# Kernel optimization log

Hardware: AMD Instinct MI355X
Metric: run time of the kernel (lower is better)

The kernel has to match this reference:

```python
import jax, jax.numpy as jnp
import numpy as np

N = 8192      # total packed vision tokens
D = 1280      # hidden_size
H = 16        # num_heads
K = 80        # head_dim = D // H
M = 16        # number of image segments
LMAX = 1024   # static upper bound on per-image segment length
SCALE = K ** (-0.5)
NEG = -1e30   # finite mask value (avoids NaN on fully-padded rows)


def _rotate_half(x):
    h = x.shape[-1] // 2
    return jnp.concatenate([-x[..., h:], x[..., :h]], axis=-1)


def setup_inputs() -> dict:
    key = jax.random.key(0)
    ks = jax.random.split(key, 5)
    hidden = jax.random.normal(ks[0], (N, D), jnp.float32)
    # ragged per-image lengths (sum == N, each <= LMAX)
    lengths = np.array([256, 768] * (M // 2), dtype=np.int32)
    cu = jnp.asarray(np.concatenate([[0], np.cumsum(lengths)]).astype(np.int32))
    # rotary tables, shape (N, head_dim)
    inv_freq = 1.0 / (10000.0 ** (np.arange(0, K, 2, dtype=np.float32) / K))  # (K/2,)
    freqs = np.arange(N, dtype=np.float32)[:, None] * inv_freq[None, :]       # (N, K/2)
    emb = np.concatenate([freqs, freqs], axis=-1)                              # (N, K)
    cos = jnp.asarray(np.cos(emb), jnp.float32)
    sin = jnp.asarray(np.sin(emb), jnp.float32)
    W_qkv = jax.random.normal(ks[1], (D, 3 * D), jnp.float32) * (D ** -0.5)
    b_qkv = jax.random.normal(ks[2], (3 * D,), jnp.float32) * 0.01
    W_proj = jax.random.normal(ks[3], (D, D), jnp.float32) * (D ** -0.5)
    b_proj = jax.random.normal(ks[4], (D,), jnp.float32) * 0.01
    return dict(hidden_ND=hidden, cu_seqlens=cu, cos_NK=cos, sin_NK=sin,
                W_qkv=W_qkv, b_qkv=b_qkv, W_proj=W_proj, b_proj=b_proj)


def reference(hidden_ND, cu_seqlens, cos_NK, sin_NK, W_qkv, b_qkv, W_proj, b_proj):
    n = hidden_ND.shape[0]
    # fused QKV projection
    qkv = (hidden_ND @ W_qkv + b_qkv).reshape(n, 3, H, K)
    q, k, v = qkv[:, 0], qkv[:, 1], qkv[:, 2]          # (N, H, K)
    # inline RoPE on Q/K (fp32 math, as in apply_rotary_pos_emb_vision)
    cos = cos_NK[:, None, :]
    sin = sin_NK[:, None, :]
    q = q * cos + _rotate_half(q) * sin
    k = k * cos + _rotate_half(k) * sin
    # gather packed tokens into padded per-segment blocks (honors segment sparsity:
    # no cross-segment tiles are ever materialized)
    lengths = jnp.diff(cu_seqlens)                                  # (M,)
    idx = cu_seqlens[:-1, None] + jnp.arange(LMAX)[None, :]         # (M, LMAX)
    valid = jnp.arange(LMAX)[None, :] < lengths[:, None]            # (M, LMAX)
    idxc = jnp.minimum(idx, n - 1)
    qg, kg, vg = q[idxc], k[idxc], v[idxc]                          # (M, LMAX, H, K)
    # per-segment attention
    scores = jnp.einsum('mqhd,mkhd->mhqk', qg, kg) * SCALE          # (M, H, LMAX, LMAX)
    mask = valid[:, None, :, None] & valid[:, None, None, :]
    scores = jnp.where(mask, scores, NEG)
    p = jax.nn.softmax(scores, axis=-1)
    og = jnp.einsum('mhqk,mkhd->mqhd', p, vg)                       # (M, LMAX, H, K)
    # scatter back to packed layout: token n -> (segment, position)
    seg = jnp.searchsorted(cu_seqlens[1:], jnp.arange(n), side='right')
    pos = jnp.arange(n) - cu_seqlens[seg]
    attn_ND = og[seg, pos].reshape(n, H * K)
    return attn_ND @ W_proj + b_proj
```

## Files before the change

kernel.cpp:

```cpp
#include <hip/hip_runtime.h>
#include <hip/hip_bf16.h>
#include <stdint.h>

#define NTOK 8192
#define DMODEL 1280
#define NHEAD 16
#define HDIM 80
#define NSEG 16
#define SCALE_F 0.11180339887498949f
#define NEG_F -1e30f

typedef __bf16 bf16x8 __attribute__((ext_vector_type(8)));
typedef float f32x4 __attribute__((ext_vector_type(4)));

__device__ __forceinline__ void gload_lds16(const void* g, void* l) {
  __builtin_amdgcn_global_load_lds((__attribute__((address_space(1))) void*)g,
                                   (__attribute__((address_space(3))) void*)l,
                                   16, 0, 0);
}

__global__ __launch_bounds__(256)
void cvt_f32_to_bf16(const float* __restrict__ src, __hip_bfloat16* __restrict__ dst) {
  int i = (blockIdx.x * 256 + threadIdx.x) * 4;
  float4 v = *(const float4*)(src + i);
  __align__(8) __hip_bfloat16 o[4] = {__float2bfloat16(v.x), __float2bfloat16(v.y),
                                      __float2bfloat16(v.z), __float2bfloat16(v.w)};
  *(uint2*)(dst + i) = *(const uint2*)o;
}

__global__ __launch_bounds__(256)
void transpose_w(const float* __restrict__ src, __hip_bfloat16* __restrict__ dst,
                 int R, int C) {
  __shared__ __hip_bfloat16 tile[32][33];
  int c0 = blockIdx.x * 32, r0 = blockIdx.y * 32;
  int tx = threadIdx.x & 31, ty = threadIdx.x >> 5;
#pragma unroll
  for (int i = 0; i < 4; ++i) {
    int r = ty + i * 8;
    tile[r][tx] = __float2bfloat16(src[(size_t)(r0 + r) * C + c0 + tx]);
  }
  __syncthreads();
#pragma unroll
  for (int i = 0; i < 4; ++i) {
    int r = ty + i * 8;
    dst[(size_t)(c0 + r) * R + r0 + tx] = tile[tx][r];
  }
}

__global__ __launch_bounds__(256)
void rope2(__hip_bfloat16* __restrict__ qkv,
           const float* __restrict__ cosb, const float* __restrict__ sinb) {
  int t = blockIdx.x * 256 + threadIdx.x;
  int p = t % 5;
  int rest = t / 5;
  int h = rest & 15;
  int qk = (rest >> 4) & 1;
  int n = rest >> 5;
  size_t base = (size_t)n * 3840 + qk * 1280 + h * 80 + p * 8;
  const float* cb = cosb + n * 80 + p * 8;
  const float* sb = sinb + n * 80 + p * 8;
  float4 cA = *(const float4*)cb, cB = *(const float4*)(cb + 4);
  float4 cC = *(const float4*)(cb + 40), cD = *(const float4*)(cb + 44);
  float4 sA = *(const float4*)sb, sB = *(const float4*)(sb + 4);
  float4 sC = *(const float4*)(sb + 40), sD = *(const float4*)(sb + 44);
  float c0[8] = {cA.x, cA.y, cA.z, cA.w, cB.x, cB.y, cB.z, cB.w};
  float c1[8] = {cC.x, cC.y, cC.z, cC.w, cD.x, cD.y, cD.z, cD.w};
  float s0[8] = {sA.x, sA.y, sA.z, sA.w, sB.x, sB.y, sB.z, sB.w};
  float s1[8] = {sC.x, sC.y, sC.z, sC.w, sD.x, sD.y, sD.z, sD.w};
  uint4 lou = *(const uint4*)(qkv + base);
  uint4 hiu = *(const uint4*)(qkv + base + 40);
  __align__(16) __hip_bfloat16 lo[8], hh[8], olo[8], ohi[8];
  *(uint4*)lo = lou; *(uint4*)hh = hiu;
#pragma unroll
  for (int e = 0; e < 8; ++e) {
    float x0 = __bfloat162float(lo[e]);
    float x1 = __bfloat162float(hh[e]);
    olo[e] = __float2bfloat16(x0 * c0[e] - x1 * s0[e]);
    ohi[e] = __float2bfloat16(x1 * c1[e] + x0 * s1[e]);
  }
  *(uint4*)(qkv + base) = *(const uint4*)olo;
  *(uint4*)(qkv + base + 40) = *(const uint4*)ohi;
}

template <bool OUT_F32, bool A_F32>
__global__ __launch_bounds__(256)
void gemm128(const void* __restrict__ Av, int lda,
             const __hip_bfloat16* __restrict__ Bt,
             const float* __restrict__ bias,
             void* __restrict__ Cv, int M, int N, int K) {
  __shared__ __align__(16) __hip_bfloat16 lds[8192];
  const int tid = threadIdx.x;
  const int lane = tid & 63;
  const int wave = tid >> 6;
  const int wr = wave >> 1, wc = wave & 1;
  const int lr = lane & 15;
  const int hi = lane >> 4;
  const int sw = (lr >> 1) & 3;
  const int lk = (hi ^ sw) << 3;
  const int m0 = blockIdx.x * 128;
  const int n0 = blockIdx.y * 128;

  f32x4 zero = {0.f, 0.f, 0.f, 0.f};
  f32x4 acc[4][4];
#pragma unroll
  for (int i = 0; i < 4; ++i)
#pragma unroll
    for (int j = 0; j < 4; ++j) acc[i][j] = zero;

  for (int k0 = 0; k0 < K; k0 += 32) {
#pragma unroll
    for (int j = 0; j < 2; ++j) {
      int v = j * 256 + tid;
      int row = v >> 2;
      int cb = ((v & 3) ^ ((v >> 3) & 3)) << 3;
      gload_lds16(Bt + (size_t)(n0 + row) * K + k0 + cb,
                  &lds[4096 + wave * 512 + j * 2048]);
    }
    if constexpr (A_F32) {
      const float* A32 = (const float*)Av;
      float4 vv[4];
#pragma unroll
      for (int j = 0; j < 4; ++j) {
        int task = j * 256 + tid;
        int row = task >> 3, cc = task & 7;
        vv[j] = *(const float4*)(A32 + (size_t)(m0 + row) * lda + k0 + cc * 4);
      }
#pragma unroll
      for (int j = 0; j < 4; ++j) {
        int task = j * 256 + tid;
        int row = task >> 3, cc = task & 7;
        int s = (cc >> 1) ^ ((row >> 1) & 3);
        __align__(8) __hip_bfloat16 t[4] = {
            __float2bfloat16(vv[j].x), __float2bfloat16(vv[j].y),
            __float2bfloat16(vv[j].z), __float2bfloat16(vv[j].w)};
        *(uint2*)&lds[row * 32 + s * 8 + (cc & 1) * 4] = *(const uint2*)t;
      }
    } else {
      const __hip_bfloat16* Abf = (const __hip_bfloat16*)Av;
#pragma unroll
      for (int j = 0; j < 2; ++j) {
        int v = j * 256 + tid;
        int row = v >> 2;
        int cb = ((v & 3) ^ ((v >> 3) & 3)) << 3;
        gload_lds16(Abf + (size_t)(m0 + row) * lda + k0 + cb,
                    &lds[wave * 512 + j * 2048]);
      }
    }
    __syncthreads();

    bf16x8 af[4], bfr[4];
#pragma unroll
    for (int i = 0; i < 4; ++i) {
      af[i]  = *(const bf16x8*)&lds[(wr * 64 + i * 16 + lr) * 32 + lk];
      bfr[i] = *(const bf16x8*)&lds[4096 + (wc * 64 + i * 16 + lr) * 32 + lk];
    }
#pragma unroll
    for (int i = 0; i < 4; ++i)
#pragma unroll
      for (int j = 0; j < 4; ++j)
        acc[i][j] = __builtin_amdgcn_mfma_f32_16x16x32_bf16(af[i], bfr[j], acc[i][j], 0, 0, 0);
    __syncthreads();
  }

  const int r0 = (lane >> 4) << 2;
#pragma unroll
  for (int j = 0; j < 4; ++j) {
    int col = n0 + wc * 64 + j * 16 + lr;
    float bv = bias[col];
#pragma unroll
    for (int i = 0; i < 4; ++i) {
      int rowb = m0 + wr * 64 + i * 16 + r0;
#pragma unroll
      for (int r = 0; r < 4; ++r) {
        float val = acc[i][j][r] + bv;
        if (OUT_F32)
          ((float*)Cv)[(size_t)(rowb + r) * N + col] = val;
        else
          ((__hip_bfloat16*)Cv)[(size_t)(rowb + r) * N + col] = __float2bfloat16(val);
      }
    }
  }
}

__global__ __launch_bounds__(512, 2)
void gemm256(const __hip_bfloat16* __restrict__ A,
             const __hip_bfloat16* __restrict__ Bt,
             const float* __restrict__ bias,
             __hip_bfloat16* __restrict__ C, int M, int N, int K) {
  __shared__ __align__(16) __hip_bfloat16 lds[49152];
  const int tid = threadIdx.x;
  const int lane = tid & 63;
  const int wave = tid >> 6;
  const int wr = wave >> 2;
  const int wc = wave & 3;
  const int lr = lane & 15;
  const int hi = lane >> 4;
  const int sw = (lr >> 1) & 3;
  const int lk = (hi ^ sw) << 3;
  const int m0 = blockIdx.x * 256;
  const int n0 = blockIdx.y * 256;

  const int scol = ((tid & 3) ^ ((tid >> 3) & 3)) * 8;
  const __hip_bfloat16* srcA = A + (size_t)(m0 + (tid >> 2)) * K + scol;
  const __hip_bfloat16* srcB = Bt + (size_t)(n0 + (tid >> 2)) * K + scol;
  const size_t row128 = (size_t)128 * K;

  auto stageA = [&](int kt, int b) {
    const __hip_bfloat16* s = srcA + kt * 32;
    gload_lds16(s,          &lds[b * 16384 + tid * 8]);
    gload_lds16(s + row128, &lds[b * 16384 + 4096 + tid * 8]);
  };
  auto stageB = [&](int kt, int b) {
    const __hip_bfloat16* s = srcB + kt * 32;
    gload_lds16(s,          &lds[b * 16384 + 8192 + tid * 8]);
    gload_lds16(s + row128, &lds[b * 16384 + 8192 + 4096 + tid * 8]);
  };

  f32x4 acc[8][4];
  f32x4 fz = {0.f, 0.f, 0.f, 0.f};
#pragma unroll
  for (int i = 0; i < 8; ++i)
#pragma unroll
    for (int j = 0; j < 4; ++j) acc[i][j] = fz;

  const int nkt = K >> 5;
  stageA(0, 0); stageB(0, 0);
  stageA(1, 1); stageB(1, 1);
  asm volatile("s_waitcnt vmcnt(4)" ::: "memory");
  __builtin_amdgcn_sched_barrier(0);
  __builtin_amdgcn_s_barrier();

  for (int t = 0; t < nkt; ++t) {
    const int b = t % 3;
    const int bs = (t + 2) % 3;
    const int ktn = (t + 2 < nkt) ? t + 2 : nkt - 1;
    const __hip_bfloat16* Ab = &lds[b * 16384 + (wr * 128) * 32];
    const __hip_bfloat16* Bb = &lds[b * 16384 + 8192 + (wc * 64) * 32];

    bf16x8 bf[4], af[4];
#pragma unroll
    for (int j = 0; j < 4; ++j) bf[j] = *(const bf16x8*)&Bb[(j * 16 + lr) * 32 + lk];
#pragma unroll
    for (int i = 0; i < 4; ++i) af[i] = *(const bf16x8*)&Ab[(i * 16 + lr) * 32 + lk];
    stageA(ktn, bs);
    __builtin_amdgcn_sched_barrier(0);
    __builtin_amdgcn_s_barrier();
    asm volatile("s_waitcnt lgkmcnt(0)" ::: "memory");
    __builtin_amdgcn_sched_barrier(0);
    __builtin_amdgcn_s_setprio(1);
#pragma unroll
    for (int i = 0; i < 4; ++i)
#pragma unroll
      for (int j = 0; j < 4; ++j)
        acc[i][j] = __builtin_amdgcn_mfma_f32_16x16x32_bf16(af[i], bf[j], acc[i][j], 0, 0, 0);
    __builtin_amdgcn_s_setprio(0);
    __builtin_amdgcn_sched_barrier(0);
    __builtin_amdgcn_s_barrier();

#pragma unroll
    for (int i = 0; i < 4; ++i) af[i] = *(const bf16x8*)&Ab[((i + 4) * 16 + lr) * 32 + lk];
    stageB(ktn, bs);
    asm volatile("s_waitcnt vmcnt(4)" ::: "memory");
    __builtin_amdgcn_sched_barrier(0);
    __builtin_amdgcn_s_barrier();
    asm volatile("s_waitcnt lgkmcnt(0)" ::: "memory");
    __builtin_amdgcn_sched_barrier(0);
    __builtin_amdgcn_s_setprio(1);
#pragma unroll
    for (int i = 0; i < 4; ++i)
#pragma unroll
      for (int j = 0; j < 4; ++j)
        acc[4 + i][j] = __builtin_amdgcn_mfma_f32_16x16x32_bf16(af[i], bf[j], acc[4 + i][j], 0, 0, 0);
    __builtin_amdgcn_s_setprio(0);
    __builtin_amdgcn_sched_barrier(0);
    __builtin_amdgcn_s_barrier();
  }

#pragma unroll
  for (int j = 0; j < 4; ++j) {
    int col = n0 + wc * 64 + j * 16 + lr;
    float bv = bias[col];
#pragma unroll
    for (int i = 0; i < 8; ++i) {
      int row0 = m0 + wr * 128 + i * 16 + hi * 4;
#pragma unroll
      for (int r = 0; r < 4; ++r)
        C[(size_t)(row0 + r) * N + col] = __float2bfloat16(acc[i][j][r] + bv);
    }
  }
}

__global__ __launch_bounds__(256, 3)
void attn_fwd(__hip_bfloat16* __restrict__ qkv, const int* __restrict__ cu) {
  const int bid = blockIdx.x;
  const int l = (bid & 7) * 288 + (bid >> 3);
  const int h = l / 144;
  const int pid = l - h * 144;
  int seg = -1, qt = 0, start = 0, L = 0;
  int accq = 0;
#pragma unroll 1
  for (int s2 = 0; s2 < NSEG; ++s2) {
    int st = cu[s2], en = cu[s2 + 1];
    int len = en - st;
    int nq = (len + 63) >> 6;
    if (seg < 0 && pid < accq + nq) { seg = s2; qt = pid - accq; start = st; L = len; }
    accq += nq;
  }
  if (seg < 0) return;

  __shared__ __align__(16) __hip_bfloat16 Ks[2][64 * 80];
  __shared__ __align__(16) __hip_bfloat16 Vs[2][80 * 72];
  __shared__ __align__(16) __hip_bfloat16 Ps[4][16 * 72];

  const int tid = threadIdx.x;
  const int lane = tid & 63;
  const int wave = tid >> 6;
  const int lr = lane & 15;
  const int hi = lane >> 4;
  const int lk = hi * 8;
  const int nt = (L + 63) >> 6;

  bf16x8 aq[3];
  {
    bf16x8 z;
#pragma unroll
    for (int e = 0; e < 8; ++e) z[e] = (__bf16)0.0f;
    int qr = qt * 64 + wave * 16 + lr;
    if (qr > L - 1) qr = L - 1;
    const __hip_bfloat16* qp = qkv + (size_t)(start + qr) * 3840 + h * 80;
    bf16x8 a0 = *(const bf16x8*)(qp + lk);
    bf16x8 a1 = *(const bf16x8*)(qp + 32 + lk);
    bf16x8 a2 = (hi < 2) ? *(const bf16x8*)(qp + 64 + lk) : z;
#pragma unroll
    for (int e = 0; e < 8; ++e) {
      a0[e] = (__bf16)((float)a0[e] * SCALE_F);
      a1[e] = (__bf16)((float)a1[e] * SCALE_F);
      a2[e] = (__bf16)((float)a2[e] * SCALE_F);
    }
    aq[0] = a0; aq[1] = a1; aq[2] = a2;
  }

  const __hip_bfloat16* kbase = qkv + (size_t)start * 3840 + 1280 + h * 80;
  const __hip_bfloat16* vbase = qkv + (size_t)start * 3840 + 2560 + h * 80;

  auto stageK = [&](int t, int buf) {
#pragma unroll
    for (int j = 0; j < 3; ++j) {
      int i = wave + 4 * j;
      if (i < 10) {
        int E = i * 512 + lane * 8;
        int r = E / 80;
        int c = E - r * 80;
        int g = t * 64 + r;
        if (g > L - 1) g = L - 1;
        gload_lds16(kbase + (size_t)g * 3840 + c, (char*)&Ks[buf][0] + i * 1024);
      }
    }
  };
  uint4 vr[3];
  auto loadV = [&](int t) {
    int g = t * 64 + lane;
    if (g > L - 1) g = L - 1;
    size_t roff = (size_t)g * 3840;
#pragma unroll
    for (int j = 0; j < 3; ++j) {
      int c = wave + 4 * j;
      if (c < 10) vr[j] = *(const uint4*)(vbase + roff + c * 8);
    }
  };
  auto writeV = [&](int buf) {
#pragma unroll
    for (int j = 0; j < 3; ++j) {
      int c = wave + 4 * j;
      if (c < 10) {
        __align__(16) __hip_bfloat16 tmp[8];
        *(uint4*)tmp = vr[j];
#pragma unroll
        for (int e = 0; e < 8; ++e) Vs[buf][(c * 8 + e) * 72 + lane] = tmp[e];
      }
    }
  };

  float m_run[4], l_part[4];
  f32x4 fz = {0.f, 0.f, 0.f, 0.f};
  f32x4 accO[5];
#pragma unroll
  for (int r = 0; r < 4; ++r) { m_run[r] = NEG_F; l_part[r] = 0.f; }
#pragma unroll
  for (int d = 0; d < 5; ++d) accO[d] = fz;

  stageK(0, 0);
  loadV(0);
  writeV(0);
  loadV(nt > 1 ? 1 : 0);
  __syncthreads();

  int cur = 0;
  for (int t = 0; t < nt; ++t) {
    const bool more = (t + 1 < nt);
    if (more) {
      stageK(t + 1, cur ^ 1);
      writeV(cur ^ 1);
      loadV(t + 2 < nt ? t + 2 : nt - 1);
    }

    f32x4 s[4] = {fz, fz, fz, fz};
#pragma unroll
    for (int ks = 0; ks < 3; ++ks) {
#pragma unroll
      for (int j = 0; j < 4; ++j) {
        bf16x8 bk = *(const bf16x8*)&Ks[cur][(j * 16 + lr) * 80 + ks * 32 + lk];
        s[j] = __builtin_amdgcn_mfma_f32_16x16x32_bf16(aq[ks], bk, s[j], 0, 0, 0);
      }
    }
    if (t * 64 + 64 > L) {
#pragma unroll
      for (int j = 0; j < 4; ++j) {
        bool vj = (t * 64 + j * 16 + lr) < L;
#pragma unroll
        for (int r = 0; r < 4; ++r)
          s[j][r] = vj ? s[j][r] : NEG_F;
      }
    }
    float mx[4];
    bool need = false;
#pragma unroll
    for (int r = 0; r < 4; ++r) {
      mx[r] = fmaxf(fmaxf(s[0][r], s[1][r]), fmaxf(s[2][r], s[3][r]));
      need |= mx[r] > m_run[r] + 8.0f;
    }
    if (__any(need)) {
#pragma unroll
      for (int off = 1; off < 16; off <<= 1)
#pragma unroll
        for (int r = 0; r < 4; ++r)
          mx[r] = fmaxf(mx[r], __shfl_xor(mx[r], off, 64));
#pragma unroll
      for (int r = 0; r < 4; ++r) {
        float mn = fmaxf(m_run[r], mx[r]);
        float sf = __expf(m_run[r] - mn);
        m_run[r] = mn;
        l_part[r] *= sf;
#pragma unroll
        for (int d = 0; d < 5; ++d) accO[d][r] *= sf;
      }
    }
#pragma unroll
    for (int r = 0; r < 4; ++r) {
      float a0 = __expf(s[0][r] - m_run[r]); s[0][r] = a0;
      float a1 = __expf(s[1][r] - m_run[r]); s[1][r] = a1;
      float a2 = __expf(s[2][r] - m_run[r]); s[2][r] = a2;
      float a3 = __expf(s[3][r] - m_run[r]); s[3][r] = a3;
      l_part[r] += (a0 + a1) + (a2 + a3);
    }

    __hip_bfloat16* pw = &Ps[wave][0];
#pragma unroll
    for (int j = 0; j < 4; ++j)
#pragma unroll
      for (int r = 0; r < 4; ++r)
        pw[(hi * 4 + r) * 72 + j * 16 + lr] = __float2bfloat16(s[j][r]);
    asm volatile("s_waitcnt lgkmcnt(0)" ::: "memory");
    __builtin_amdgcn_sched_barrier(0);
    bf16x8 ap0 = *(const bf16x8*)&pw[lr * 72 + lk];
    bf16x8 ap1 = *(const bf16x8*)&pw[lr * 72 + 32 + lk];
#pragma unroll
    for (int d = 0; d < 5; ++d) {
      bf16x8 bv0 = *(const bf16x8*)&Vs[cur][(d * 16 + lr) * 72 + lk];
      bf16x8 bv1 = *(const bf16x8*)&Vs[cur][(d * 16 + lr) * 72 + 32 + lk];
      accO[d] = __builtin_amdgcn_mfma_f32_16x16x32_bf16(ap0, bv0, accO[d], 0, 0, 0);
      accO[d] = __builtin_amdgcn_mfma_f32_16x16x32_bf16(ap1, bv1, accO[d], 0, 0, 0);
    }

    __syncthreads();
    cur ^= 1;
  }

#pragma unroll
  for (int off = 1; off < 16; off <<= 1)
#pragma unroll
    for (int r = 0; r < 4; ++r)
      l_part[r] += __shfl_xor(l_part[r], off, 64);
  float rl[4];
#pragma unroll
  for (int r = 0; r < 4; ++r) rl[r] = 1.0f / l_part[r];
#pragma unroll
  for (int d = 0; d < 5; ++d)
#pragma unroll
    for (int r = 0; r < 4; ++r) {
      int row = qt * 64 + wave * 16 + hi * 4 + r;
      if (row < L)
        qkv[(size_t)(start + row) * 3840 + h * 80 + d * 16 + lr] =
            __float2bfloat16(accO[d][r] * rl[r]);
    }
}

extern "C" void kernel_launch(void* const* d_in, const int* in_sizes, int n_in,
                              void* d_out, int out_size, void* d_ws, size_t ws_size,
                              hipStream_t stream) {
  const float* hidden = (const float*)d_in[0];
  const int*   cu     = (const int*)d_in[1];
  const float* cosb   = (const float*)d_in[2];
  const float* sinb   = (const float*)d_in[3];
  const float* Wqkv   = (const float*)d_in[4];
  const float* bqkv   = (const float*)d_in[5];
  const float* Wproj  = (const float*)d_in[6];
  const float* bproj  = (const float*)d_in[7];
  float* out = (float*)d_out;
  char* ws = (char*)d_ws;

  __hip_bfloat16* qkv    = (__hip_bfloat16*)(ws);
  __hip_bfloat16* wqkvT  = (__hip_bfloat16*)(ws + 62914560);
  __hip_bfloat16* wprojT = (__hip_bfloat16*)(ws + 72744960);
  __hip_bfloat16* hbf    = (__hip_bfloat16*)(ws + 76021760);
  const bool use_hbf = ws_size >= (size_t)96993280;

  transpose_w<<<dim3(120, 40), 256, 0, stream>>>(Wqkv, wqkvT, 1280, 3840);
  transpose_w<<<dim3(40, 40), 256, 0, stream>>>(Wproj, wprojT, 1280, 1280);
  if (use_hbf) {
    cvt_f32_to_bf16<<<10240, 256, 0, stream>>>(hidden, hbf);
    gemm256<<<dim3(32, 15), 512, 0, stream>>>(hbf, wqkvT, bqkv, qkv, 8192, 3840, 1280);
  } else {
    gemm128<false, true><<<dim3(64, 30), 256, 0, stream>>>(hidden, 1280, wqkvT, bqkv, qkv, 8192, 3840, 1280);
  }
  rope2<<<5120, 256, 0, stream>>>(qkv, cosb, sinb);
  attn_fwd<<<2304, 256, 0, stream>>>(qkv, cu);
  gemm128<true, false><<<dim3(64, 10), 256, 0, stream>>>(qkv, 3840, wprojT, bproj, out, 8192, 1280, 1280);
}
```

Baseline: 255.3 us.

## Shrink gemm256 tile to 256x128 with double buffering and reuse it for output projection

Changes the big GEMM kernel from a 256x256 triple-buffered tile to a 256x128 double-buffered tile with a 4x2 wave layout and half the accumulators. This allows four blocks per CU and doubles the grid for the QKV projection. The kernel is templated on output type with an lda parameter so it can also replace gemm128 for the output projection. The goal is better occupancy and latency hiding. The cost is less operand reuse per tile and a full vmcnt(0) wait every k-step, which exposes load latency.

```diff
diff --git a/kernel.cpp b/kernel.cpp
--- a/kernel.cpp
+++ b/kernel.cpp
@@ -182,67 +182,61 @@
   }
 }
 
-__global__ __launch_bounds__(512, 2)
-void gemm256(const __hip_bfloat16* __restrict__ A,
+template <bool OUT_F32>
+__global__ __launch_bounds__(512, 4)
+void gemm256(const __hip_bfloat16* __restrict__ A, int lda,
              const __hip_bfloat16* __restrict__ Bt,
              const float* __restrict__ bias,
-             __hip_bfloat16* __restrict__ C, int M, int N, int K) {
-  __shared__ __align__(16) __hip_bfloat16 lds[49152];
+             void* __restrict__ Cv, int M, int N, int K) {
+  __shared__ __align__(16) __hip_bfloat16 lds[2][12288];
   const int tid = threadIdx.x;
   const int lane = tid & 63;
   const int wave = tid >> 6;
-  const int wr = wave >> 2;
-  const int wc = wave & 3;
+  const int wr = wave >> 1;
+  const int wc = wave & 1;
   const int lr = lane & 15;
   const int hi = lane >> 4;
-  const int sw = (lr >> 1) & 3;
-  const int lk = (hi ^ sw) << 3;
+  const int lk = (hi ^ ((lr >> 1) & 3)) << 3;
   const int m0 = blockIdx.x * 256;
-  const int n0 = blockIdx.y * 256;
+  const int n0 = blockIdx.y * 128;
 
   const int scol = ((tid & 3) ^ ((tid >> 3) & 3)) * 8;
-  const __hip_bfloat16* srcA = A + (size_t)(m0 + (tid >> 2)) * K + scol;
+  const __hip_bfloat16* srcA = A + (size_t)(m0 + (tid >> 2)) * lda + scol;
   const __hip_bfloat16* srcB = Bt + (size_t)(n0 + (tid >> 2)) * K + scol;
-  const size_t row128 = (size_t)128 * K;
-
-  auto stageA = [&](int kt, int b) {
-    const __hip_bfloat16* s = srcA + kt * 32;
-    gload_lds16(s,          &lds[b * 16384 + tid * 8]);
-    gload_lds16(s + row128, &lds[b * 16384 + 4096 + tid * 8]);
+  const size_t rowA128 = (size_t)128 * lda;
+
+  auto stage = [&](int kt, int b) {
+    const __hip_bfloat16* sa = srcA + kt * 32;
+    gload_lds16(sa,           &lds[b][tid * 8]);
+    gload_lds16(sa + rowA128, &lds[b][4096 + tid * 8]);
+    gload_lds16(srcB + kt * 32, &lds[b][8192 + tid * 8]);
   };
-  auto stageB = [&](int kt, int b) {
-    const __hip_bfloat16* s = srcB + kt * 32;
-    gload_lds16(s,          &lds[b * 16384 + 8192 + tid * 8]);
-    gload_lds16(s + row128, &lds[b * 16384 + 8192 + 4096 + tid * 8]);
-  };
-
-  f32x4 acc[8][4];
+
+  f32x4 acc[4][4];
   f32x4 fz = {0.f, 0.f, 0.f, 0.f};
 #pragma unroll
-  for (int i = 0; i < 8; ++i)
+  for (int i = 0; i < 4; ++i)
 #pragma unroll
     for (int j = 0; j < 4; ++j) acc[i][j] = fz;
 
   const int nkt = K >> 5;
-  stageA(0, 0); stageB(0, 0);
-  stageA(1, 1); stageB(1, 1);
-  asm volatile("s_waitcnt vmcnt(4)" ::: "memory");
+  stage(0, 0);
+  asm volatile("s_waitcnt vmcnt(0)" ::: "memory");
   __builtin_amdgcn_sched_barrier(0);
   __builtin_amdgcn_s_barrier();
 
   for (int t = 0; t < nkt; ++t) {
-    const int b = t % 3;
-    const int bs = (t + 2) % 3;
-    const int ktn = (t + 2 < nkt) ? t + 2 : nkt - 1;
-    const __hip_bfloat16* Ab = &lds[b * 16384 + (wr * 128) * 32];
-    const __hip_bfloat16* Bb = &lds[b * 16384 + 8192 + (wc * 64) * 32];
-
-    bf16x8 bf[4], af[4];
+    const int b = t & 1;
+    const int ktn = (t + 1 < nkt) ? t + 1 : nkt - 1;
+    const __hip_bfloat16* Ab = &lds[b][(wr * 64) * 32];
+    const __hip_bfloat16* Bb = &lds[b][8192 + (wc * 64) * 32];
+
+    bf16x8 af[4], bf[4];
+#pragma unroll
+    for (int i = 0; i < 4; ++i) af[i] = *(const bf16x8*)&Ab[(i * 16 + lr) * 32 + lk];
 #pragma unroll
     for (int j = 0; j < 4; ++j) bf[j] = *(const bf16x8*)&Bb[(j * 16 + lr) * 32 + lk];
-#pragma unroll
-    for (int i = 0; i < 4; ++i) af[i] = *(const bf16x8*)&Ab[(i * 16 + lr) * 32 + lk];
-    stageA(ktn, bs);
+    stage(ktn, b ^ 1);
     __builtin_amdgcn_sched_barrier(0);
     __builtin_amdgcn_s_barrier();
     asm volatile("s_waitcnt lgkmcnt(0)" ::: "memory");
@@ -255,23 +249,7 @@
         acc[i][j] = __builtin_amdgcn_mfma_f32_16x16x32_bf16(af[i], bf[j], acc[i][j], 0, 0, 0);
     __builtin_amdgcn_s_setprio(0);
     __builtin_amdgcn_sched_barrier(0);
-    __builtin_amdgcn_s_barrier();
-
-#pragma unroll
-    for (int i = 0; i < 4; ++i) af[i] = *(const bf16x8*)&Ab[((i + 4) * 16 + lr) * 32 + lk];
-    stageB(ktn, bs);
-    asm volatile("s_waitcnt vmcnt(4)" ::: "memory");
-    __builtin_amdgcn_sched_barrier(0);
-    __builtin_amdgcn_s_barrier();
-    asm volatile("s_waitcnt lgkmcnt(0)" ::: "memory");
-    __builtin_amdgcn_sched_barrier(0);
-    __builtin_amdgcn_s_setprio(1);
-#pragma unroll
-    for (int i = 0; i < 4; ++i)
-#pragma unroll
-      for (int j = 0; j < 4; ++j)
-        acc[4 + i][j] = __builtin_amdgcn_mfma_f32_16x16x32_bf16(af[i], bf[j], acc[4 + i][j], 0, 0, 0);
-    __builtin_amdgcn_s_setprio(0);
+    asm volatile("s_waitcnt vmcnt(0)" ::: "memory");
     __builtin_amdgcn_sched_barrier(0);
     __builtin_amdgcn_s_barrier();
   }
@@ -281,11 +259,16 @@
     int col = n0 + wc * 64 + j * 16 + lr;
     float bv = bias[col];
 #pragma unroll
-    for (int i = 0; i < 8; ++i) {
-      int row0 = m0 + wr * 128 + i * 16 + hi * 4;
-#pragma unroll
-      for (int r = 0; r < 4; ++r)
-        C[(size_t)(row0 + r) * N + col] = __float2bfloat16(acc[i][j][r] + bv);
+    for (int i = 0; i < 4; ++i) {
+      int row0 = m0 + wr * 64 + i * 16 + hi * 4;
+#pragma unroll
+      for (int r = 0; r < 4; ++r) {
+        float val = acc[i][j][r] + bv;
+        if (OUT_F32)
+          ((float*)Cv)[(size_t)(row0 + r) * N + col] = val;
+        else
+          ((__hip_bfloat16*)Cv)[(size_t)(row0 + r) * N + col] = __float2bfloat16(val);
+      }
     }
   }
 }
@@ -519,11 +502,11 @@
   transpose_w<<<dim3(40, 40), 256, 0, stream>>>(Wproj, wprojT, 1280, 1280);
   if (use_hbf) {
     cvt_f32_to_bf16<<<10240, 256, 0, stream>>>(hidden, hbf);
-    gemm256<<<dim3(32, 15), 512, 0, stream>>>(hbf, wqkvT, bqkv, qkv, 8192, 3840, 1280);
+    gemm256<false><<<dim3(32, 30), 512, 0, stream>>>(hbf, 1280, wqkvT, bqkv, qkv, 8192, 3840, 1280);
   } else {
     gemm128<false, true><<<dim3(64, 30), 256, 0, stream>>>(hidden, 1280, wqkvT, bqkv, qkv, 8192, 3840, 1280);
   }
   rope2<<<5120, 256, 0, stream>>>(qkv, cosb, sinb);
   attn_fwd<<<2304, 256, 0, stream>>>(qkv, cu);
-  gemm128<true, false><<<dim3(64, 10), 256, 0, stream>>>(qkv, 3840, wprojT, bproj, out, 8192, 1280, 1280);
-}
+  gemm256<true><<<dim3(32, 10), 512, 0, stream>>>(qkv, 3840, wprojT, bproj, out, 8192, 1280, 1280);
+}
```

After: 246.4 us. 3.5% less time.
